# Kernel tuning notes

Hardware: AMD Instinct MI355X
Metric: run time of the kernel (lower is better)

The kernel has to match this reference:

```python
import jax, jax.numpy as jnp
import numpy as np

B, N, E, H = 4, 2048, 1024, 16
D = E // H  # head dim = 64


def setup_inputs() -> dict:
    key = jax.random.key(0)
    k1, k2, k3 = jax.random.split(key, 3)
    x = jax.random.normal(k1, (B, N, E), dtype=jnp.float32)
    # torch nn.Linear weights are [out_features, in_features]
    w_qkv = jax.random.normal(k2, (3 * E, E), dtype=jnp.float32) * (E ** -0.5)
    w_out = jax.random.normal(k3, (E, E), dtype=jnp.float32) * (E ** -0.5)
    return {"x": x, "w_qkv": w_qkv, "w_out": w_out}


def reference(x, w_qkv, w_out):
    # fused QKV projection: [B,N,E] @ [E,3E] -> [B,N,3E]
    qkv = jnp.einsum("bne,fe->bnf", x, w_qkv)
    q, k, v = jnp.split(qkv, 3, axis=-1)
    # b n (h d) -> b h n d
    split_heads = lambda t: t.reshape(B, N, H, D).transpose(0, 2, 1, 3)
    q, k, v = map(split_heads, (q, k, v))
    scale = D ** -0.5
    scores = jnp.einsum("bhnd,bhmd->bhnm", q, k) * scale
    attn = jax.nn.softmax(scores, axis=-1)
    out = jnp.einsum("bhnm,bhmd->bhnd", attn, v)
    # b h n d -> b n (h d)
    out = out.transpose(0, 2, 1, 3).reshape(B, N, E)
    return jnp.einsum("bne,fe->bnf", out, w_out)
```

## Files before the change

kernel.cpp:

```cpp
#include <hip/hip_runtime.h>
#include <hip/hip_bf16.h>

typedef short bf16x8 __attribute__((ext_vector_type(8)));
typedef float f32x4 __attribute__((ext_vector_type(4)));
using bf16 = __hip_bfloat16;

#define MFMA16(a, b, c) __builtin_amdgcn_mfma_f32_16x16x32_bf16(a, b, c, 0, 0, 0)

typedef unsigned int u32;
typedef u32 __attribute__((address_space(1))) global_u32;
typedef u32 __attribute__((address_space(3))) lds_u32;

__device__ __forceinline__ void gload_lds16(const unsigned short* g, unsigned short* l) {
    __builtin_amdgcn_global_load_lds((const global_u32*)g, (lds_u32*)l, 16, 0, 0);
}

__device__ __forceinline__ short f2b(float f) {
    __hip_bfloat16 h = __float2bfloat16(f);
    return *reinterpret_cast<short*>(&h);
}

__global__ __launch_bounds__(256) void cvt3_kernel(const float* __restrict__ x,
                                                   const float* __restrict__ wq,
                                                   const float* __restrict__ wo,
                                                   unsigned short* __restrict__ xb,
                                                   unsigned short* __restrict__ wqb,
                                                   unsigned short* __restrict__ wob) {
    const int id = blockIdx.x;
    const float* src;
    unsigned short* dst;
    size_t off;
    if (id < 4096) {
        src = x; dst = xb; off = (size_t)id * 2048;
    } else if (id < 5632) {
        src = wq; dst = wqb; off = (size_t)(id - 4096) * 2048;
    } else {
        src = wo; dst = wob; off = (size_t)(id - 5632) * 2048;
    }
    const size_t i = off + (size_t)threadIdx.x * 8;
    float4 v0 = *(const float4*)(src + i);
    float4 v1 = *(const float4*)(src + i + 4);
    bf16x8 o;
    o[0] = f2b(v0.x); o[1] = f2b(v0.y); o[2] = f2b(v0.z); o[3] = f2b(v0.w);
    o[4] = f2b(v1.x); o[5] = f2b(v1.y); o[6] = f2b(v1.z); o[7] = f2b(v1.w);
    *(bf16x8*)(dst + i) = o;
}

template <int MODE>
__global__ __launch_bounds__(256) void gemm128_kernel(const unsigned short* __restrict__ A,
                                                      const unsigned short* __restrict__ W,
                                                      void* __restrict__ outp) {
    __shared__ unsigned short As[128][64];
    __shared__ unsigned short Ws[128][64];
    const int tid = threadIdx.x;
    const int lane = tid & 63;
    const int w = tid >> 6;
    const int wr = w >> 1, wc = w & 1;
    const int lm = lane & 15, quad = lane >> 4;
    const int m0 = blockIdx.y * 128, n0 = blockIdx.x * 128;

    const int srow8 = lane >> 3;
    const int skg = (lane & 7) ^ srow8;
    const unsigned short* Ag = A + (size_t)(m0 + w * 32 + srow8) * 1024 + skg * 8;
    const unsigned short* Wg = W + (size_t)(n0 + w * 32 + srow8) * 1024 + skg * 8;

    f32x4 acc[4][4] = {};

    for (int k0 = 0; k0 < 1024; k0 += 64) {
        __syncthreads();
#pragma unroll
        for (int j = 0; j < 4; j++) {
            gload_lds16(Ag + j * (8 * 1024), &As[w * 32 + j * 8][0]);
            gload_lds16(Wg + j * (8 * 1024), &Ws[w * 32 + j * 8][0]);
        }
        Ag += 64;
        Wg += 64;
        __syncthreads();
#pragma unroll
        for (int ks = 0; ks < 2; ks++) {
            const int swz = ((quad + ks * 4) ^ (lm & 7)) * 8;
            bf16x8 af[4], bf[4];
#pragma unroll
            for (int mt = 0; mt < 4; mt++)
                af[mt] = *(const bf16x8*)&As[wr * 64 + mt * 16 + lm][swz];
#pragma unroll
            for (int nt = 0; nt < 4; nt++)
                bf[nt] = *(const bf16x8*)&Ws[wc * 64 + nt * 16 + lm][swz];
#pragma unroll
            for (int mt = 0; mt < 4; mt++)
#pragma unroll
                for (int nt = 0; nt < 4; nt++)
                    acc[mt][nt] = MFMA16(af[mt], bf[nt], acc[mt][nt]);
        }
    }

#pragma unroll
    for (int mt = 0; mt < 4; mt++)
#pragma unroll
        for (int nt = 0; nt < 4; nt++) {
            f32x4 v = acc[mt][nt];
            const int gr0 = m0 + wr * 64 + mt * 16 + quad * 4;
            const int gc = n0 + wc * 64 + nt * 16 + lm;
            if (MODE == 2) {
                bf16* qkv = (bf16*)outp;
                const int which = gc >> 10;
                const int h = (gc >> 6) & 15;
                const int d = gc & 63;
                const int b = gr0 >> 11, n = gr0 & 2047;
                if (which == 2) {
                    short4 pk;
                    pk.x = f2b(v[0]); pk.y = f2b(v[1]); pk.z = f2b(v[2]); pk.w = f2b(v[3]);
                    *(short4*)&qkv[2ull * 8388608 +
                                   ((size_t)((b * 16 + h) * 64 + d)) * 2048 + n] = pk;
                } else {
#pragma unroll
                    for (int r = 0; r < 4; r++) {
                        float val = v[r];
                        if (which == 0) val *= 0.125f;
                        qkv[(size_t)which * 8388608 +
                            ((size_t)((b * 16 + h) * 2048 + n + r)) * 64 + d] =
                            __float2bfloat16(val);
                    }
                }
            } else {
                float* o = (float*)outp;
#pragma unroll
                for (int r = 0; r < 4; r++) o[(size_t)(gr0 + r) * 1024 + gc] = v[r];
            }
        }
}

__global__ __launch_bounds__(512, 2) void gemm256x128_qkv_kernel(
    const unsigned short* __restrict__ A,
    const unsigned short* __restrict__ W,
    unsigned short* __restrict__ qkvp) {
    __shared__ unsigned short As[2][256][64];
    __shared__ unsigned short Bs[2][128][64];
    const int tid = threadIdx.x;
    const int lane = tid & 63;
    const int w = tid >> 6;
    const int wr = w >> 1, wc = w & 1;
    const int lm = lane & 15, quad = lane >> 4;

    const int id = blockIdx.x;
    const int xs = (id & 7) * 96 + (id >> 3);
    const int n0 = (xs % 24) * 128;
    const int m0 = (xs / 24) * 256;

    const int sr = lane >> 3;
    const int sg = (lane & 7) ^ sr;
    const unsigned short* Ab = A + (size_t)(m0 + w * 8 + sr) * 1024 + sg * 8;
    const unsigned short* Wb = W + (size_t)(n0 + w * 8 + sr) * 1024 + sg * 8;

    f32x4 acc[4][4] = {};
    bf16x8 af[2][2];
    bf16x8 bfA[2][2];
    bf16x8 bfB[2][2];

#define STAGE_A(buf, half, kk)                                                     \
    do {                                                                           \
        gload_lds16(Ab + (size_t)((half) * 128) * 1024 + (kk),                     \
                    &As[buf][(half) * 128 + w * 8][0]);                            \
        gload_lds16(Ab + (size_t)((half) * 128 + 64) * 1024 + (kk),                \
                    &As[buf][(half) * 128 + 64 + w * 8][0]);                       \
    } while (0)
#define STAGE_B(buf, kk)                                                           \
    do {                                                                           \
        gload_lds16(Wb + (kk), &Bs[buf][w * 8][0]);                                \
        gload_lds16(Wb + (size_t)64 * 1024 + (kk), &Bs[buf][64 + w * 8][0]);       \
    } while (0)
#define LDA(buf, mh)                                                               \
    do {                                                                           \
        _Pragma("unroll") for (int mt2 = 0; mt2 < 2; mt2++)                        \
            _Pragma("unroll") for (int ks = 0; ks < 2; ks++)                       \
                af[mt2][ks] =                                                      \
                    *(const bf16x8*)&As[buf][wr * 64 + ((mh) * 2 + mt2) * 16 + lm] \
                                        [(((quad + ks * 4) ^ (lm & 7)) * 8)];      \
    } while (0)
#define LDB(buf, nh, DST)                                                          \
    do {                                                                           \
        _Pragma("unroll") for (int nt2 = 0; nt2 < 2; nt2++)                        \
            _Pragma("unroll") for (int ks = 0; ks < 2; ks++)                       \
                DST[nt2][ks] =                                                     \
                    *(const bf16x8*)&Bs[buf][wc * 64 + ((nh) * 2 + nt2) * 16 + lm] \
                                        [(((quad + ks * 4) ^ (lm & 7)) * 8)];      \
    } while (0)
#define PHASE_MM(mh, nh, BF)                                                       \
    do {                                                                           \
        __builtin_amdgcn_s_barrier();                                              \
        asm volatile("s_waitcnt lgkmcnt(0)" ::: "memory");                         \
        __builtin_amdgcn_s_setprio(1);                                             \
        _Pragma("unroll") for (int mt2 = 0; mt2 < 2; mt2++)                        \
            _Pragma("unroll") for (int nt2 = 0; nt2 < 2; nt2++) {                  \
                f32x4 t0 = MFMA16(af[mt2][0], BF[nt2][0],                          \
                                  acc[(mh) * 2 + mt2][(nh) * 2 + nt2]);            \
                acc[(mh) * 2 + mt2][(nh) * 2 + nt2] =                              \
                    MFMA16(af[mt2][1], BF[nt2][1], t0);                            \
            }                                                                      \
        __builtin_amdgcn_s_setprio(0);                                             \
        __builtin_amdgcn_s_barrier();                                              \
    } while (0)
#define VMCNT2 asm volatile("s_waitcnt vmcnt(2)" ::: "memory")

    STAGE_A(0, 0, 0); STAGE_A(0, 1, 0);
    STAGE_B(0, 0);
    STAGE_B(1, 64);
    VMCNT2;
    __builtin_amdgcn_s_barrier();

    for (int i = 0; i < 8; i++) {
        const int t = 2 * i;
        const int k1 = (t + 1) * 64;
        const int k2 = (t + 2 < 16) ? (t + 2) * 64 : 0;
        const int k3 = (t + 3 < 16) ? (t + 3) * 64 : 0;
        LDA(0, 0); LDB(0, 0, bfA);
        STAGE_A(1, 0, k1);
        PHASE_MM(0, 0, bfA);
        LDB(0, 1, bfB);
        STAGE_A(1, 1, k1);
        PHASE_MM(0, 1, bfB);
        LDA(0, 1);
        STAGE_B(0, k2);
        PHASE_MM(1, 1, bfB);
        VMCNT2;
        PHASE_MM(1, 0, bfA);
        LDA(1, 0); LDB(1, 0, bfA);
        STAGE_A(0, 0, k2);
        PHASE_MM(0, 0, bfA);
        LDB(1, 1, bfB);
        STAGE_A(0, 1, k2);
        PHASE_MM(0, 1, bfB);
        LDA(1, 1);
        STAGE_B(1, k3);
        PHASE_MM(1, 1, bfB);
        VMCNT2;
        PHASE_MM(1, 0, bfA);
    }

    asm volatile("s_waitcnt vmcnt(0)" ::: "memory");

    bf16* qkv = (bf16*)qkvp;
#pragma unroll
    for (int mt = 0; mt < 4; mt++)
#pragma unroll
        for (int nt = 0; nt < 4; nt++) {
            f32x4 v = acc[mt][nt];
            const int gr0 = m0 + wr * 64 + mt * 16 + quad * 4;
            const int gc = n0 + wc * 64 + nt * 16 + lm;
            const int which = gc >> 10;
            const int h = (gc >> 6) & 15;
            const int d = gc & 63;
            const int b = gr0 >> 11, n = gr0 & 2047;
            if (which == 2) {
                short4 pk;
                pk.x = f2b(v[0]); pk.y = f2b(v[1]); pk.z = f2b(v[2]); pk.w = f2b(v[3]);
                *(short4*)&qkv[2ull * 8388608 +
                               ((size_t)((b * 16 + h) * 64 + d)) * 2048 + n] = pk;
            } else {
#pragma unroll
                for (int r = 0; r < 4; r++) {
                    float val = v[r];
                    if (which == 0) val *= 0.125f;
                    qkv[(size_t)which * 8388608 +
                        ((size_t)((b * 16 + h) * 2048 + n + r)) * 64 + d] =
                        __float2bfloat16(val);
                }
            }
        }
#undef STAGE_A
#undef STAGE_B
#undef LDA
#undef LDB
#undef PHASE_MM
#undef VMCNT2
}

__global__ __launch_bounds__(256, 4) void attn_mfma_kernel(
    const unsigned short* __restrict__ Qg, const unsigned short* __restrict__ Kg,
    const unsigned short* __restrict__ Vtg, unsigned short* __restrict__ O) {
    __shared__ unsigned short Ks[64][64];
    __shared__ unsigned short Vs[64][64];
    __shared__ unsigned short Ps[4][2][16][64];
    const int tid = threadIdx.x;
    const int lane = tid & 63;
    const int w = tid >> 6;
    const int lm = lane & 15;
    const int quad = lane >> 4;
    const int bh = blockIdx.x & 63;
    const int n0 = (blockIdx.x >> 6) * 128;
    const size_t base = (size_t)bh * (2048 * 64);

    bf16x8 qf[2][2];
#pragma unroll
    for (int mt = 0; mt < 2; mt++)
#pragma unroll
        for (int ks = 0; ks < 2; ks++)
            qf[mt][ks] = *(const bf16x8*)&Qg[base +
                                            (size_t)(n0 + w * 32 + mt * 16 + lm) * 64 +
                                            ks * 32 + quad * 8];

    f32x4 accO[2][4] = {};
    float lst[2] = {0.f, 0.f};

    const int sr = lane >> 3;
    const int sg = (lane & 7) ^ sr;

    for (int t = 0; t < 32; t++) {
        const int k0 = t * 64;
        __syncthreads();
#pragma unroll
        for (int j = 0; j < 2; j++) {
            const int row = w * 16 + j * 8 + sr;
            gload_lds16(&Kg[base + (size_t)(k0 + row) * 64 + sg * 8], &Ks[w * 16 + j * 8][0]);
            gload_lds16(&Vtg[base + (size_t)row * 2048 + k0 + sg * 8], &Vs[w * 16 + j * 8][0]);
        }
        __syncthreads();

        bf16x8 kb[4][2];
#pragma unroll
        for (int kt = 0; kt < 4; kt++)
#pragma unroll
            for (int ks = 0; ks < 2; ks++)
                kb[kt][ks] = *(const bf16x8*)&Ks[kt * 16 + lm]
                                               [(((ks * 4 + quad) ^ (lm & 7)) * 8)];
        f32x4 s[2][4];
#pragma unroll
        for (int mt = 0; mt < 2; mt++)
#pragma unroll
            for (int kt = 0; kt < 4; kt++) {
                f32x4 z = {};
                z = MFMA16(kb[kt][0], qf[mt][0], z);
                s[mt][kt] = MFMA16(kb[kt][1], qf[mt][1], z);
            }

#pragma unroll
        for (int mt = 0; mt < 2; mt++) {
            float ps = 0.f;
#pragma unroll
            for (int kt = 0; kt < 4; kt++) {
                const float p0 = __expf(s[mt][kt][0]);
                const float p1 = __expf(s[mt][kt][1]);
                const float p2 = __expf(s[mt][kt][2]);
                const float p3 = __expf(s[mt][kt][3]);
                ps += (p0 + p1) + (p2 + p3);
                short4 pk;
                pk.x = f2b(p0); pk.y = f2b(p1); pk.z = f2b(p2); pk.w = f2b(p3);
                const int g = kt * 2 + (quad >> 1);
                *(short4*)&Ps[w][mt][lm][((g ^ (lm & 7)) * 8) + (quad & 1) * 4] = pk;
            }
            lst[mt] += ps;
        }

        bf16x8 vbf[4][2];
#pragma unroll
        for (int nt = 0; nt < 4; nt++)
#pragma unroll
            for (int ks = 0; ks < 2; ks++)
                vbf[nt][ks] = *(const bf16x8*)&Vs[nt * 16 + lm]
                                                [(((ks * 4 + quad) ^ (lm & 7)) * 8)];
#pragma unroll
        for (int mt = 0; mt < 2; mt++) {
            bf16x8 pb0 = *(const bf16x8*)&Ps[w][mt][lm][(((quad) ^ (lm & 7)) * 8)];
            bf16x8 pb1 = *(const bf16x8*)&Ps[w][mt][lm][(((4 + quad) ^ (lm & 7)) * 8)];
#pragma unroll
            for (int nt = 0; nt < 4; nt++) {
                f32x4 a = MFMA16(vbf[nt][0], pb0, accO[mt][nt]);
                accO[mt][nt] = MFMA16(vbf[nt][1], pb1, a);
            }
        }
    }

#pragma unroll
    for (int mt = 0; mt < 2; mt++) {
        lst[mt] += __shfl_xor(lst[mt], 16);
        lst[mt] += __shfl_xor(lst[mt], 32);
    }

    const int b = bh >> 4, h = bh & 15;
#pragma unroll
    for (int mt = 0; mt < 2; mt++) {
        const float inv = 1.0f / lst[mt];
        const int n = n0 + w * 32 + mt * 16 + lm;
#pragma unroll
        for (int nt = 0; nt < 4; nt++) {
            short4 pk;
            pk.x = f2b(accO[mt][nt][0] * inv);
            pk.y = f2b(accO[mt][nt][1] * inv);
            pk.z = f2b(accO[mt][nt][2] * inv);
            pk.w = f2b(accO[mt][nt][3] * inv);
            *(short4*)&O[((size_t)(b * 2048 + n)) * 1024 + h * 64 + nt * 16 + quad * 4] = pk;
        }
    }
}

extern "C" void kernel_launch(void* const* d_in, const int* in_sizes, int n_in,
                              void* d_out, int out_size, void* d_ws, size_t ws_size,
                              hipStream_t stream) {
    const float* x = (const float*)d_in[0];
    const float* w_qkv = (const float*)d_in[1];
    const float* w_out = (const float*)d_in[2];
    float* out = (float*)d_out;

    unsigned short* qkvb = (unsigned short*)d_ws;
    unsigned short* xb = qkvb + 3ull * 8388608;
    unsigned short* wqkvb = xb + 8388608;
    unsigned short* woutb = wqkvb + 3145728;

    cvt3_kernel<<<6144, 256, 0, stream>>>(x, w_qkv, w_out, xb, wqkvb, woutb);
    gemm256x128_qkv_kernel<<<768, 512, 0, stream>>>(xb, wqkvb, qkvb);
    attn_mfma_kernel<<<1024, 256, 0, stream>>>(qkvb, qkvb + 8388608,
                                               qkvb + 2 * 8388608, xb);
    gemm128_kernel<1><<<dim3(8, 64), 256, 0, stream>>>(xb, woutb, out);
}
```

Baseline: 262.9 us.

## Double-buffer K tiles, overlap V load with QK^T, use native exp2

The attention loop now double-buffers K in shared memory. The next K tile is prefetched while the current one is used, and the V load overlaps the QK^T and exp work, with split waitcnt and barrier points. The softmax scale is folded into Q together with log2(e) so the kernel can call the hardware v_exp_f32 (exp2) directly instead of __expf. MFMA sections are wrapped in s_setprio hints. The costs are extra LDS per block, which may affect occupancy at 4 blocks per CU, and more delicate vmcnt-based synchronisation.

```diff
diff --git a/kernel.cpp b/kernel.cpp
--- a/kernel.cpp
+++ b/kernel.cpp
@@ -19,6 +19,14 @@
     __hip_bfloat16 h = __float2bfloat16(f);
     return *reinterpret_cast<short*>(&h);
 }
+
+__device__ __forceinline__ float exp2_fast(float x) {
+    float r;
+    asm("v_exp_f32 %0, %1" : "=v"(r) : "v"(x));
+    return r;
+}
+
+#define QSCALE 0.18033688011112042f
 
 __global__ __launch_bounds__(256) void cvt3_kernel(const float* __restrict__ x,
                                                    const float* __restrict__ wq,
@@ -116,7 +124,7 @@
 #pragma unroll
                     for (int r = 0; r < 4; r++) {
                         float val = v[r];
-                        if (which == 0) val *= 0.125f;
+                        if (which == 0) val *= QSCALE;
                         qkv[(size_t)which * 8388608 +
                             ((size_t)((b * 16 + h) * 2048 + n + r)) * 64 + d] =
                             __float2bfloat16(val);
@@ -260,7 +268,7 @@
 #pragma unroll
                 for (int r = 0; r < 4; r++) {
                     float val = v[r];
-                    if (which == 0) val *= 0.125f;
+                    if (which == 0) val *= QSCALE;
                     qkv[(size_t)which * 8388608 +
                         ((size_t)((b * 16 + h) * 2048 + n + r)) * 64 + d] =
                         __float2bfloat16(val);
@@ -278,7 +286,7 @@
 __global__ __launch_bounds__(256, 4) void attn_mfma_kernel(
     const unsigned short* __restrict__ Qg, const unsigned short* __restrict__ Kg,
     const unsigned short* __restrict__ Vtg, unsigned short* __restrict__ O) {
-    __shared__ unsigned short Ks[64][64];
+    __shared__ unsigned short Ks[2][64][64];
     __shared__ unsigned short Vs[64][64];
     __shared__ unsigned short Ps[4][2][16][64];
     const int tid = threadIdx.x;
@@ -305,43 +313,59 @@
     const int sr = lane >> 3;
     const int sg = (lane & 7) ^ sr;
 
+#pragma unroll
+    for (int j = 0; j < 2; j++) {
+        const int row = w * 16 + j * 8 + sr;
+        gload_lds16(&Kg[base + (size_t)row * 64 + sg * 8], &Ks[0][w * 16 + j * 8][0]);
+    }
+    asm volatile("s_waitcnt vmcnt(0)" ::: "memory");
+    __builtin_amdgcn_s_barrier();
+
+    int kb = 0;
     for (int t = 0; t < 32; t++) {
         const int k0 = t * 64;
-        __syncthreads();
+        const int k0n = (t + 1 < 32) ? (t + 1) * 64 : 0;
 #pragma unroll
         for (int j = 0; j < 2; j++) {
             const int row = w * 16 + j * 8 + sr;
-            gload_lds16(&Kg[base + (size_t)(k0 + row) * 64 + sg * 8], &Ks[w * 16 + j * 8][0]);
-            gload_lds16(&Vtg[base + (size_t)row * 2048 + k0 + sg * 8], &Vs[w * 16 + j * 8][0]);
-        }
-        __syncthreads();
-
-        bf16x8 kb[4][2];
+            gload_lds16(&Vtg[base + (size_t)row * 2048 + k0 + sg * 8],
+                        &Vs[w * 16 + j * 8][0]);
+        }
+#pragma unroll
+        for (int j = 0; j < 2; j++) {
+            const int row = w * 16 + j * 8 + sr;
+            gload_lds16(&Kg[base + (size_t)(k0n + row) * 64 + sg * 8],
+                        &Ks[kb ^ 1][w * 16 + j * 8][0]);
+        }
+
+        bf16x8 kbf[4][2];
 #pragma unroll
         for (int kt = 0; kt < 4; kt++)
 #pragma unroll
             for (int ks = 0; ks < 2; ks++)
-                kb[kt][ks] = *(const bf16x8*)&Ks[kt * 16 + lm]
-                                               [(((ks * 4 + quad) ^ (lm & 7)) * 8)];
+                kbf[kt][ks] = *(const bf16x8*)&Ks[kb][kt * 16 + lm]
+                                                 [(((ks * 4 + quad) ^ (lm & 7)) * 8)];
         f32x4 s[2][4];
+        __builtin_amdgcn_s_setprio(1);
 #pragma unroll
         for (int mt = 0; mt < 2; mt++)
 #pragma unroll
             for (int kt = 0; kt < 4; kt++) {
                 f32x4 z = {};
-                z = MFMA16(kb[kt][0], qf[mt][0], z);
-                s[mt][kt] = MFMA16(kb[kt][1], qf[mt][1], z);
+                z = MFMA16(kbf[kt][0], qf[mt][0], z);
+                s[mt][kt] = MFMA16(kbf[kt][1], qf[mt][1], z);
             }
+        __builtin_amdgcn_s_setprio(0);
 
 #pragma unroll
         for (int mt = 0; mt < 2; mt++) {
             float ps = 0.f;
 #pragma unroll
             for (int kt = 0; kt < 4; kt++) {
-                const float p0 = __expf(s[mt][kt][0]);
-                const float p1 = __expf(s[mt][kt][1]);
-                const float p2 = __expf(s[mt][kt][2]);
-                const float p3 = __expf(s[mt][kt][3]);
+                const float p0 = exp2_fast(s[mt][kt][0]);
+                const float p1 = exp2_fast(s[mt][kt][1]);
+                const float p2 = exp2_fast(s[mt][kt][2]);
+                const float p3 = exp2_fast(s[mt][kt][3]);
                 ps += (p0 + p1) + (p2 + p3);
                 short4 pk;
                 pk.x = f2b(p0); pk.y = f2b(p1); pk.z = f2b(p2); pk.w = f2b(p3);
@@ -351,6 +375,9 @@
             lst[mt] += ps;
         }
 
+        asm volatile("s_waitcnt vmcnt(2)" ::: "memory");
+        __builtin_amdgcn_s_barrier();
+
         bf16x8 vbf[4][2];
 #pragma unroll
         for (int nt = 0; nt < 4; nt++)
@@ -358,6 +385,7 @@
             for (int ks = 0; ks < 2; ks++)
                 vbf[nt][ks] = *(const bf16x8*)&Vs[nt * 16 + lm]
                                                 [(((ks * 4 + quad) ^ (lm & 7)) * 8)];
+        __builtin_amdgcn_s_setprio(1);
 #pragma unroll
         for (int mt = 0; mt < 2; mt++) {
             bf16x8 pb0 = *(const bf16x8*)&Ps[w][mt][lm][(((quad) ^ (lm & 7)) * 8)];
@@ -368,6 +396,11 @@
                 accO[mt][nt] = MFMA16(vbf[nt][1], pb1, a);
             }
         }
+        __builtin_amdgcn_s_setprio(0);
+
+        asm volatile("s_waitcnt vmcnt(0)" ::: "memory");
+        __builtin_amdgcn_s_barrier();
+        kb ^= 1;
     }
 
 #pragma unroll
```

Result: no change. 264.4 us (+0.6%).
